# Performance work log

Measured on AMD Instinct MI355X. Metric: run time of the kernel, lower is better.

The kernel has to match this reference:

```python
import jax, jax.numpy as jnp
import numpy as np

GAMMA = 0.2
B, C, K = 2048, 32000, 8
BIG = 1e8


def setup_inputs() -> dict:
    key = jax.random.key(0)
    k1, k2, k3 = jax.random.split(key, 3)
    x = jax.random.normal(k1, (B, C), dtype=jnp.float32)
    y = jax.random.randint(k2, (B, K), 0, C, dtype=jnp.int32)
    neg = jax.random.uniform(k3, (B, K)) < 0.3
    neg = neg.at[:, 0].set(False)
    y = jnp.where(neg, jnp.int32(-1), y)
    return {"x": x, "y": y}


def _forward(x, y):
    Bn, Cn = x.shape
    target = y[:, 0]
    # loss1: standard mean cross-entropy on primary label
    logp = jax.nn.log_softmax(x, axis=1)
    loss1 = -jnp.mean(jnp.take_along_axis(logp, target[:, None].astype(jnp.int32), axis=1))
    pos_mask = y != -1                                   # [B, K]
    sample_mask = jnp.sum(pos_mask, axis=1) > 1          # rows with >1 positive label
    y_safe = jnp.where(pos_mask, y, 0)
    # gather logits at all positive labels; padding slots get +BIG so argmin/min ignores them
    pos_data = jnp.where(pos_mask, jnp.take_along_axis(x, y_safe, axis=1), BIG)
    min_rel = jnp.min(pos_data, axis=1, keepdims=True)   # [B, 1] = min positive logit
    # scatter -BIG into x at every positive label position (padding scatters add 0 at col 0)
    row = jnp.arange(Bn, dtype=jnp.int32)[:, None]
    hit = jnp.zeros((Bn, Cn), jnp.int32).at[row, y_safe].add(pos_mask.astype(jnp.int32))
    new_x = jnp.where(hit > 0, -BIG, x)                  # positives suppressed
    # relative CE: min positive logit (class 0) vs. all non-positive logits
    rel = jnp.concatenate([min_rel, new_x], axis=1)      # [B, C+1]
    ce2 = -jax.nn.log_softmax(rel, axis=1)[:, 0]
    cnt = jnp.sum(sample_mask.astype(x.dtype))
    loss2 = jnp.sum(jnp.where(sample_mask, ce2, jnp.zeros_like(ce2))) / jnp.maximum(cnt, 1.0)
    return loss1 + GAMMA * loss2


def reference(x, y):
    return _forward(x, y)
```

## Files before the change

### kernel.cpp

```cpp
#include <hip/hip_runtime.h>
#include <math.h>

#define GAMMA 0.2f
#define BN 2048
#define CN 32000
#define KN 8
#define BIGV 100000000.0f

typedef float fx4 __attribute__((ext_vector_type(4)));

#define EXP4(v) ((__expf((v)[0]) + __expf((v)[1])) + (__expf((v)[2]) + __expf((v)[3])))

__global__ __launch_bounds__(256) void row_kernel(const float* __restrict__ x,
                                                  const int* __restrict__ y,
                                                  float4* __restrict__ row_out) {
    const int blk = blockIdx.x;
    const int tid = threadIdx.x;
    const int r0 = 2 * blk;
    const float* xrow0 = x + (size_t)r0 * CN;
    const float* xrow1 = xrow0 + CN;
    const fx4* xr0 = (const fx4*)xrow0;
    const fx4* xr1 = (const fx4*)xrow1;

    __shared__ int s_y[2][KN];
    __shared__ float s_xv[2][KN];
    __shared__ float ss[4][2];

    if (tid < 2 * KN) {
        const int r = tid >> 3, k = tid & 7;
        const int yk = y[(r0 + r) * KN + k];
        s_y[r][k] = yk;
        s_xv[r][k] = x[(size_t)(r0 + r) * CN + (yk == -1 ? 0 : yk)];
    }

    float a0 = 0.f, a1 = 0.f, b0 = 0.f, b1 = 0.f;
    #pragma unroll
    for (int it = 0; it < 28; it += 2) {
        fx4 p = xr0[tid + (it + 0) * 256];
        fx4 q = xr1[tid + (it + 0) * 256];
        fx4 r = xr0[tid + (it + 1) * 256];
        fx4 t = xr1[tid + (it + 1) * 256];
        a0 += EXP4(p);
        b0 += EXP4(q);
        a1 += EXP4(r);
        b1 += EXP4(t);
    }
    #pragma unroll
    for (int it = 28; it < 31; ++it) {
        fx4 p = xr0[tid + it * 256];
        fx4 q = xr1[tid + it * 256];
        a0 += EXP4(p);
        b0 += EXP4(q);
    }
    if (tid < 64) {
        fx4 p = xr0[tid + 31 * 256];
        fx4 q = xr1[tid + 31 * 256];
        a1 += EXP4(p);
        b1 += EXP4(q);
    }
    float sa = a0 + a1;
    float sb = b0 + b1;

    #pragma unroll
    for (int off = 1; off < 64; off <<= 1) {
        sa += __shfl_xor(sa, off);
        sb += __shfl_xor(sb, off);
    }
    const int wave = tid >> 6;
    if ((tid & 63) == 0) { ss[wave][0] = sa; ss[wave][1] = sb; }
    __syncthreads();

    if (tid < 2) {
        const float S = (ss[0][tid] + ss[1][tid]) + (ss[2][tid] + ss[3][tid]);
        const float loss1 = logf(S) - s_xv[tid][0];

        int yv[KN];
        #pragma unroll
        for (int k = 0; k < KN; ++k) yv[k] = s_y[tid][k];

        int npos = 0;
        float min_rel = BIGV;
        float sum_hit = 0.f;
        #pragma unroll
        for (int k = 0; k < KN; ++k) {
            if (yv[k] != -1) {
                ++npos;
                const float xv = s_xv[tid][k];
                min_rel = fminf(min_rel, xv);
                bool dup = false;
                for (int j = 0; j < k; ++j) dup = dup || (yv[j] == yv[k]);
                if (!dup) sum_hit += __expf(xv);
            }
        }
        float ce2 = 0.f, msk = 0.f;
        if (npos > 1) {
            const float rest = fmaxf(S - sum_hit, 0.f);
            ce2 = logf(__expf(min_rel) + rest) - min_rel;
            msk = 1.f;
        }
        row_out[r0 + tid] = make_float4(loss1, ce2, msk, 0.f);
    }
}

__global__ __launch_bounds__(256) void finalize_kernel(const float4* __restrict__ row_out,
                                                       float* __restrict__ out) {
    const int tid = threadIdx.x;
    float s1 = 0.f, s2 = 0.f, sc = 0.f;
    for (int i = tid; i < BN; i += 256) {
        const float4 v = row_out[i];
        s1 += v.x; s2 += v.y; sc += v.z;
    }
    #pragma unroll
    for (int off = 1; off < 64; off <<= 1) {
        s1 += __shfl_xor(s1, off);
        s2 += __shfl_xor(s2, off);
        sc += __shfl_xor(sc, off);
    }
    __shared__ float a1[4], a2[4], ac[4];
    const int wave = tid >> 6;
    if ((tid & 63) == 0) { a1[wave] = s1; a2[wave] = s2; ac[wave] = sc; }
    __syncthreads();
    if (tid == 0) {
        #pragma unroll
        for (int w = 1; w < 4; ++w) { s1 += a1[w]; s2 += a2[w]; sc += ac[w]; }
        out[0] = s1 / (float)BN + GAMMA * (s2 / fmaxf(sc, 1.0f));
    }
}

extern "C" void kernel_launch(void* const* d_in, const int* in_sizes, int n_in,
                              void* d_out, int out_size, void* d_ws, size_t ws_size,
                              hipStream_t stream) {
    const float* x = (const float*)d_in[0];
    const int* y = (const int*)d_in[1];
    float4* row_out = (float4*)d_ws;

    row_kernel<<<BN / 2, 256, 0, stream>>>(x, y, row_out);
    finalize_kernel<<<1, 256, 0, stream>>>(row_out, (float*)d_out);
}
```

Before: 48.84 us.

## Fuse final reduction into row kernel via slotted atomics and last-block finalize

Replaces the separate finalize kernel with per-block atomic accumulation into 64 padded slots plus a completion counter; the last block to finish reduces the slots and writes the output. This removes the second kernel launch and the per-row output write and read. In exchange it adds a memset on the stream, atomic traffic, and relies on a waitcnt plus counter ordering for correctness. Summation order also becomes nondeterministic.

Measured after the change: 54.98 us. 1.13x slower.

```diff
diff --git a/kernel.cpp b/kernel.cpp
--- a/kernel.cpp
+++ b/kernel.cpp
@@ -6,14 +6,17 @@
 #define CN 32000
 #define KN 8
 #define BIGV 100000000.0f
+#define SLOTS 64
 
 typedef float fx4 __attribute__((ext_vector_type(4)));
 
 #define EXP4(v) ((__expf((v)[0]) + __expf((v)[1])) + (__expf((v)[2]) + __expf((v)[3])))
 
-__global__ __launch_bounds__(256) void row_kernel(const float* __restrict__ x,
-                                                  const int* __restrict__ y,
-                                                  float4* __restrict__ row_out) {
+__global__ __launch_bounds__(256) void fused_kernel(const float* __restrict__ x,
+                                                    const int* __restrict__ y,
+                                                    float* __restrict__ acc,
+                                                    unsigned int* __restrict__ counter,
+                                                    float* __restrict__ out) {
     const int blk = blockIdx.x;
     const int tid = threadIdx.x;
     const int r0 = 2 * blk;
@@ -25,6 +28,7 @@
     __shared__ int s_y[2][KN];
     __shared__ float s_xv[2][KN];
     __shared__ float ss[4][2];
+    __shared__ bool s_last;
 
     if (tid < 2 * KN) {
         const int r = tid >> 3, k = tid & 7;
@@ -98,32 +102,35 @@
             ce2 = logf(__expf(min_rel) + rest) - min_rel;
             msk = 1.f;
         }
-        row_out[r0 + tid] = make_float4(loss1, ce2, msk, 0.f);
+
+        const float p1 = loss1 + __shfl_xor(loss1, 1);
+        const float p2 = ce2 + __shfl_xor(ce2, 1);
+        const float pc = msk + __shfl_xor(msk, 1);
+        if (tid == 0) {
+            const int slot = blk & (SLOTS - 1);
+            atomicAdd(&acc[slot * 16 + 0], p1);
+            atomicAdd(&acc[slot * 16 + 1], p2);
+            atomicAdd(&acc[slot * 16 + 2], pc);
+            asm volatile("s_waitcnt vmcnt(0)" ::: "memory");
+            const unsigned int old = atomicAdd(counter, 1u);
+            s_last = (old == (unsigned int)(gridDim.x - 1));
+        }
     }
-}
+    __syncthreads();
 
-__global__ __launch_bounds__(256) void finalize_kernel(const float4* __restrict__ row_out,
-                                                       float* __restrict__ out) {
-    const int tid = threadIdx.x;
-    float s1 = 0.f, s2 = 0.f, sc = 0.f;
-    for (int i = tid; i < BN; i += 256) {
-        const float4 v = row_out[i];
-        s1 += v.x; s2 += v.y; sc += v.z;
-    }
-    #pragma unroll
-    for (int off = 1; off < 64; off <<= 1) {
-        s1 += __shfl_xor(s1, off);
-        s2 += __shfl_xor(s2, off);
-        sc += __shfl_xor(sc, off);
-    }
-    __shared__ float a1[4], a2[4], ac[4];
-    const int wave = tid >> 6;
-    if ((tid & 63) == 0) { a1[wave] = s1; a2[wave] = s2; ac[wave] = sc; }
-    __syncthreads();
-    if (tid == 0) {
+    if (s_last && tid < SLOTS) {
+        float r1 = atomicAdd(&acc[tid * 16 + 0], 0.0f);
+        float r2 = atomicAdd(&acc[tid * 16 + 1], 0.0f);
+        float rc = atomicAdd(&acc[tid * 16 + 2], 0.0f);
         #pragma unroll
-        for (int w = 1; w < 4; ++w) { s1 += a1[w]; s2 += a2[w]; sc += ac[w]; }
-        out[0] = s1 / (float)BN + GAMMA * (s2 / fmaxf(sc, 1.0f));
+        for (int off = 1; off < 64; off <<= 1) {
+            r1 += __shfl_xor(r1, off);
+            r2 += __shfl_xor(r2, off);
+            rc += __shfl_xor(rc, off);
+        }
+        if (tid == 0) {
+            out[0] = r1 / (float)BN + GAMMA * (r2 / fmaxf(rc, 1.0f));
+        }
     }
 }
 
@@ -132,8 +139,9 @@
                               hipStream_t stream) {
     const float* x = (const float*)d_in[0];
     const int* y = (const int*)d_in[1];
-    float4* row_out = (float4*)d_ws;
+    float* acc = (float*)d_ws;
+    unsigned int* counter = (unsigned int*)((char*)d_ws + SLOTS * 16 * sizeof(float));
 
-    row_kernel<<<BN / 2, 256, 0, stream>>>(x, y, row_out);
-    finalize_kernel<<<1, 256, 0, stream>>>(row_out, (float*)d_out);
+    hipMemsetAsync(d_ws, 0, SLOTS * 16 * sizeof(float) + sizeof(unsigned int), stream);
+    fused_kernel<<<BN / 2, 256, 0, stream>>>(x, y, acc, counter, (float*)d_out);
 }
```
